# Kernel optimization log

Measured on AMD Instinct MI355X. Metric: run time of the kernel, lower is better.

Reference implementation:

```python
import math
import jax, jax.numpy as jnp
import numpy as np

D_MODEL = 1024
N_HEADS = 16
D_K = D_MODEL // N_HEADS
THETA = 10000.0
B, S = 2, 2048


def setup_inputs() -> dict:
    key = jax.random.key(0)
    k1, k2, k3 = jax.random.split(key, 3)
    x = jax.random.normal(k1, (B, S, D_MODEL), dtype=jnp.float32)
    token_positions = jnp.arange(B * S, dtype=jnp.int32).reshape(B, S)
    std_qkv = math.sqrt(2.0 / (D_MODEL + 3 * D_MODEL))
    std_o = math.sqrt(2.0 / (D_MODEL + D_MODEL))
    W_qkv = jax.random.truncated_normal(k2, -3.0, 3.0, (3 * D_MODEL, D_MODEL), dtype=jnp.float32) * std_qkv
    W_o = jax.random.truncated_normal(k3, -3.0, 3.0, (D_MODEL, D_MODEL), dtype=jnp.float32) * std_o
    return {"x": x, "W_qkv": W_qkv, "W_o": W_o, "token_positions": token_positions}


def _rope(x, pos):
    # x: (B, H, S, D_K); pos: (B, S) int
    half = D_K // 2
    inv_freq = 1.0 / (THETA ** (jnp.arange(0, D_K, 2, dtype=jnp.float32) / D_K))  # (half,)
    # pos_extended = pos[:, None, :] -> freqs (B, 1, S, half)
    freqs = pos[:, None, :, None].astype(jnp.float32) * inv_freq
    cos, sin = jnp.cos(freqs), jnp.sin(freqs)
    xr = x.reshape(*x.shape[:-1], half, 2)
    x1, x2 = xr[..., 0], xr[..., 1]
    out = jnp.stack([x1 * cos - x2 * sin, x2 * cos + x1 * sin], axis=-1)
    return out.reshape(x.shape)


def reference(x, W_qkv, W_o, token_positions):
    seq_len = x.shape[-2]
    qkv = jnp.einsum('bsi,oi->bso', x, W_qkv)
    q, k, v = jnp.split(qkv, 3, axis=-1)
    # (B, S, H*D) -> (B, H, S, D)
    def to_heads(t):
        return t.reshape(t.shape[0], t.shape[1], N_HEADS, D_K).transpose(0, 2, 1, 3)
    q, k, v = to_heads(q), to_heads(k), to_heads(v)
    q = _rope(q, token_positions)
    k = _rope(k, token_positions)
    scores = jnp.einsum('bhnd,bhmd->bhnm', q, k) / math.sqrt(D_K)
    causal = jnp.tril(jnp.ones((seq_len, seq_len), dtype=bool))
    scores = jnp.where(causal, scores, -jnp.inf)
    attn = jax.nn.softmax(scores, axis=-1)
    out = jnp.einsum('bhnm,bhmd->bhnd', attn, v)
    out = out.transpose(0, 2, 1, 3).reshape(x.shape[0], seq_len, D_MODEL)
    return jnp.einsum('bsi,oi->bso', out, W_o)
```

## Files before the change

### kernel.cpp

```cpp
#include <hip/hip_runtime.h>
#include <cmath>

typedef __bf16 bf16;
typedef bf16 bf16x4 __attribute__((ext_vector_type(4)));
typedef bf16 bf16x8 __attribute__((ext_vector_type(8)));
typedef float f32x4 __attribute__((ext_vector_type(4)));

#define MFMA16(a, b, c) __builtin_amdgcn_mfma_f32_16x16x32_bf16(a, b, c, 0, 0, 0)

__global__ __launch_bounds__(256) void cvt_all(
    const float* __restrict__ x, const float* __restrict__ wqkv,
    const float* __restrict__ wo, bf16* __restrict__ xb,
    bf16* __restrict__ wqkvb, bf16* __restrict__ wob) {
  int i = (blockIdx.x * 256 + threadIdx.x) * 4;
  const float* src;
  bf16* dst;
  if (i < (4 << 20)) {
    src = x + i; dst = xb + i;
  } else if (i < (7 << 20)) {
    src = wqkv + (i - (4 << 20)); dst = wqkvb + (i - (4 << 20));
  } else {
    src = wo + (i - (7 << 20)); dst = wob + (i - (7 << 20));
  }
  const f32x4 v = *(const f32x4*)src;
  bf16x4 o = {(bf16)v[0], (bf16)v[1], (bf16)v[2], (bf16)v[3]};
  *(bf16x4*)dst = o;
}

template <int EPI, int BN>
__global__ __launch_bounds__(256) void gemm_nt(
    const bf16* __restrict__ A, const bf16* __restrict__ Bm,
    const int* __restrict__ tokpos,
    bf16* __restrict__ out0, bf16* __restrict__ out1, bf16* __restrict__ out2,
    float* __restrict__ outF, int N) {
  constexpr int NI = BN / 32;
  __shared__ __align__(16) bf16 As[2][128 * 32];
  __shared__ __align__(16) bf16 Bs[2][BN * 32];
  const int tid = threadIdx.x;
  const int w = tid >> 6, lane = tid & 63, quad = lane >> 4, m16 = lane & 15;
  const int m0 = blockIdx.y * 128, n0 = blockIdx.x * BN;
  const int wm = (w >> 1) * 64, wn = (w & 1) * (BN / 2);

  f32x4 acc[4][NI] = {};

  const int row0 = tid >> 2, ch = tid & 3;
  const bf16* Ag0 = A + (size_t)(m0 + row0) * 1024 + ch * 8;
  const bf16* Ag1 = A + (size_t)(m0 + 64 + row0) * 1024 + ch * 8;
  const bf16* Bg0 = Bm + (size_t)(n0 + row0) * 1024 + ch * 8;
  const bf16* Bg1 =
      (BN == 128) ? Bm + (size_t)(n0 + 64 + row0) * 1024 + ch * 8 : nullptr;

  bf16x8 ra0, ra1, rb0, rb1;
  auto LOAD = [&](int k0) {
    ra0 = *(const bf16x8*)(Ag0 + k0);
    ra1 = *(const bf16x8*)(Ag1 + k0);
    rb0 = *(const bf16x8*)(Bg0 + k0);
    if constexpr (BN == 128) rb1 = *(const bf16x8*)(Bg1 + k0);
  };
  auto WRITE = [&](int p) {
    *(bf16x8*)(As[p] + tid * 8) = ra0;
    *(bf16x8*)(As[p] + 2048 + tid * 8) = ra1;
    *(bf16x8*)(Bs[p] + tid * 8) = rb0;
    if constexpr (BN == 128) *(bf16x8*)(Bs[p] + 2048 + tid * 8) = rb1;
  };

  LOAD(0);
  WRITE(0);
  __syncthreads();

  int p = 0;
  for (int k0 = 0; k0 < 1024; k0 += 32) {
    const bool more = (k0 + 32) < 1024;
    if (more) LOAD(k0 + 32);
    bf16x8 af[4], bfr[NI];
#pragma unroll
    for (int mi = 0; mi < 4; ++mi)
      af[mi] = *(const bf16x8*)(As[p] + (wm + mi * 16 + m16) * 32 + quad * 8);
#pragma unroll
    for (int ni = 0; ni < NI; ++ni)
      bfr[ni] = *(const bf16x8*)(Bs[p] + (wn + ni * 16 + m16) * 32 + quad * 8);
#pragma unroll
    for (int mi = 0; mi < 4; ++mi)
#pragma unroll
      for (int ni = 0; ni < NI; ++ni)
        acc[mi][ni] = MFMA16(af[mi], bfr[ni], acc[mi][ni]);
    if (more) {
      WRITE(1 - p);
      __syncthreads();
      p ^= 1;
    }
  }

  if constexpr (EPI == 0) {
#pragma unroll
    for (int mi = 0; mi < 4; ++mi) {
      int rowb = m0 + wm + mi * 16 + quad * 4;
#pragma unroll
      for (int r = 0; r < 4; ++r) {
        size_t off = (size_t)(rowb + r) * N + n0 + wn;
#pragma unroll
        for (int ni = 0; ni < NI; ++ni)
          outF[off + ni * 16 + m16] = acc[mi][ni][r];
      }
    }
  } else {
#pragma unroll
    for (int mi = 0; mi < 4; ++mi) {
      int rowb = m0 + wm + mi * 16 + quad * 4;
      int pos4[4];
#pragma unroll
      for (int r = 0; r < 4; ++r) pos4[r] = tokpos[rowb + r];
#pragma unroll
      for (int ni = 0; ni < NI; ++ni) {
        int col = n0 + wn + ni * 16 + m16;
        int sec = col >> 10, f = col & 1023, h = f >> 6, d = f & 63;
        if (sec == 2) {
#pragma unroll
          for (int r = 0; r < 4; ++r) {
            int row = rowb + r;
            int bb = row >> 11, s = row & 2047;
            out2[((size_t)(bb * 16 + h) * 64 + d) * 2048 + s] =
                (bf16)acc[mi][ni][r];
          }
        } else {
          float inv = __expf(-(float)(d & ~1) * (9.2103403719762f / 64.f));
          bf16* dst = sec ? out1 : out0;
          const float sc = sec ? 1.0f : 0.125f;
#pragma unroll
          for (int r = 0; r < 4; ++r) {
            float v = acc[mi][ni][r];
            float vp = __shfl_xor(v, 1);
            float ang = (float)pos4[r] * inv;
            float cs, sn;
            __sincosf(ang, &sn, &cs);
            float ov = (d & 1) ? (v * cs + vp * sn) : (v * cs - vp * sn);
            ov *= sc;
            int row = rowb + r;
            int bb = row >> 11, s = row & 2047;
            dst[((size_t)(bb * 16 + h) * 2048 + s) * 64 + d] = (bf16)ov;
          }
        }
      }
    }
  }
}

__global__ __launch_bounds__(256) void attn_kernel(
    const bf16* __restrict__ Q, const bf16* __restrict__ K,
    const bf16* __restrict__ Vt, bf16* __restrict__ O) {
  __shared__ __align__(16) bf16 KP[3][64 * 72];
  __shared__ __align__(16) bf16 VP[3][64 * 72];
  __shared__ __align__(16) bf16 PS[4][16 * 72];
  const int tid = threadIdx.x;
  const int w = tid >> 6, lane = tid & 63, quad = lane >> 4, m16 = lane & 15;
  const int bh = blockIdx.x;
  const int j = blockIdx.y;
  const int qtA = j, qtB = 31 - j;
  const int q0A = qtA * 64, q0B = qtB * 64;
  const bf16* Qb = Q + (size_t)bh * 2048 * 64;
  const bf16* Kb = K + (size_t)bh * 2048 * 64;
  const bf16* Vb = Vt + (size_t)bh * 64 * 2048;

  const int ch0 = w * 8, ch1 = (w + 4) * 8;
  const bf16* Kg = Kb + (size_t)lane * 64;
  const bf16* Vg = Vb + (size_t)lane * 2048;

  const bf16* qrowA = Qb + (size_t)(q0A + w * 16 + m16) * 64;
  const bf16* qrowB = Qb + (size_t)(q0B + w * 16 + m16) * 64;
  bf16x8 aqA[2], aqB[2];
  aqA[0] = *(const bf16x8*)(qrowA + quad * 8);
  aqA[1] = *(const bf16x8*)(qrowA + 32 + quad * 8);
  aqB[0] = *(const bf16x8*)(qrowB + quad * 8);
  aqB[1] = *(const bf16x8*)(qrowB + 32 + quad * 8);

  bf16x8 rk0, rk1, rv0, rv1;
  auto PREFETCH = [&](int kt) {
    rk0 = *(const bf16x8*)(Kg + (size_t)kt * 64 * 64 + ch0);
    rk1 = *(const bf16x8*)(Kg + (size_t)kt * 64 * 64 + ch1);
    rv0 = *(const bf16x8*)(Vg + kt * 64 + ch0);
    rv1 = *(const bf16x8*)(Vg + kt * 64 + ch1);
  };
  auto STAGE = [&](int p) {
    *(bf16x8*)(KP[p] + lane * 72 + ch0) = rk0;
    *(bf16x8*)(KP[p] + lane * 72 + ch1) = rk1;
    *(bf16x8*)(VP[p] + lane * 72 + ch0) = rv0;
    *(bf16x8*)(VP[p] + lane * 72 + ch1) = rv1;
  };

  PREFETCH(0);
  STAGE(0);
  PREFETCH(1);
  STAGE(1);
  __syncthreads();

  auto QK = [&](int p, const bf16x8* aq, f32x4* sa) {
#pragma unroll
    for (int kk = 0; kk < 2; ++kk)
#pragma unroll
      for (int ni = 0; ni < 4; ++ni) {
        bf16x8 bk = *(const bf16x8*)(KP[p] + (ni * 16 + m16) * 72 + kk * 32 +
                                     quad * 8);
        sa[ni] = MFMA16(aq[kk], bk, sa[ni]);
      }
  };

  f32x4 oA[4] = {}, oB[4] = {};
  float lA[4] = {0.f, 0.f, 0.f, 0.f}, lB[4] = {0.f, 0.f, 0.f, 0.f};
  const int qrel = w * 16 + quad * 4;

  auto SOFTPV = [&](int p, const f32x4* sa, f32x4* o, float* lp, bool diag) {
    bf16* ps = PS[w];
#pragma unroll
    for (int r = 0; r < 4; ++r) {
#pragma unroll
      for (int ni = 0; ni < 4; ++ni) {
        float pp = exp2f(fmaf(sa[ni][r], 1.44269504f, -11.5415603f));
        if (diag && (ni * 16 + m16) > qrel + r) pp = 0.f;
        lp[r] += pp;
        ps[(quad * 4 + r) * 72 + ni * 16 + m16] = (bf16)pp;
      }
    }
    bf16x8 ap[2];
    ap[0] = *(const bf16x8*)(ps + m16 * 72 + quad * 8);
    ap[1] = *(const bf16x8*)(ps + m16 * 72 + 32 + quad * 8);
#pragma unroll
    for (int kk = 0; kk < 2; ++kk)
#pragma unroll
      for (int ng = 0; ng < 4; ++ng) {
        bf16x8 bv = *(const bf16x8*)(VP[p] + (ng * 16 + m16) * 72 + kk * 32 +
                                     quad * 8);
        o[ng] = MFMA16(ap[kk], bv, o[ng]);
      }
  };

  f32x4 saA[4] = {}, saB[4] = {};
  QK(0, aqB, saB);
  QK(0, aqA, saA);

  int pc = 0, pn = 1, pst = 2;
  for (int kt = 0; kt <= qtB; ++kt) {
    const bool more = kt < qtB;
    const bool stage2 = (kt + 2) <= qtB;
    if (stage2) PREFETCH(kt + 2);

    f32x4 saBn[4] = {}, saAn[4] = {};
    if (more) QK(pn, aqB, saBn);
    if (kt + 1 <= qtA) QK(pn, aqA, saAn);

    SOFTPV(pc, saB, oB, lB, kt == qtB);
    if (kt <= qtA) SOFTPV(pc, saA, oA, lA, kt == qtA);

    if (stage2) STAGE(pst);
    if (more) __syncthreads();

#pragma unroll
    for (int i = 0; i < 4; ++i) { saB[i] = saBn[i]; saA[i] = saAn[i]; }
    int t = pc; pc = pn; pn = pst; pst = t;
  }

  const int b = bh >> 4, h = bh & 15;
  auto epilogue = [&](f32x4* o, float* lp, int q0) {
#pragma unroll
    for (int r = 0; r < 4; ++r) {
      float l = lp[r];
      l += __shfl_xor(l, 1);
      l += __shfl_xor(l, 2);
      l += __shfl_xor(l, 4);
      l += __shfl_xor(l, 8);
      float inv_l = 1.f / l;
      int s = q0 + w * 16 + quad * 4 + r;
      size_t rowoff = (size_t)(b * 2048 + s) * 1024 + h * 64;
#pragma unroll
      for (int ng = 0; ng < 4; ++ng)
        O[rowoff + ng * 16 + m16] = (bf16)(o[ng][r] * inv_l);
    }
  };
  epilogue(oA, lA, q0A);
  epilogue(oB, lB, q0B);
}

extern "C" void kernel_launch(void* const* d_in, const int* in_sizes, int n_in,
                              void* d_out, int out_size, void* d_ws, size_t ws_size,
                              hipStream_t stream) {
  (void)in_sizes; (void)n_in; (void)out_size; (void)ws_size;
  const float* x = (const float*)d_in[0];
  const float* Wqkv = (const float*)d_in[1];
  const float* Wo = (const float*)d_in[2];
  const int* tokpos = (const int*)d_in[3];
  float* out = (float*)d_out;

  const size_t NEL = (size_t)2 * 16 * 2048 * 64;
  bf16* Qws = (bf16*)d_ws;
  bf16* Kws = Qws + NEL;
  bf16* Vtw = Kws + NEL;
  bf16* Ows = Vtw + NEL;
  bf16* xb  = Ows + NEL;
  bf16* Wqkvb = xb + NEL;
  bf16* Wob = Wqkvb + (size_t)3072 * 1024;

  cvt_all<<<8192, 256, 0, stream>>>(x, Wqkv, Wo, xb, Wqkvb, Wob);

  gemm_nt<1, 128><<<dim3(24, 32), 256, 0, stream>>>(
      xb, Wqkvb, tokpos, Qws, Kws, Vtw, nullptr, 3072);
  attn_kernel<<<dim3(32, 16), 256, 0, stream>>>(Qws, Kws, Vtw, Ows);
  gemm_nt<0, 64><<<dim3(16, 32), 256, 0, stream>>>(
      Ows, Wob, nullptr, nullptr, nullptr, nullptr, out, 1024);
}
```

Measured before the change: 201.9 us.

## Split attention KV loop across two blocks and merge partials in output GEMM

Attention work is split by key tile parity (even/odd) across twice as many blocks, each writing unnormalized partial outputs and row sums. The output projection GEMM now loads both partials, sums them and divides by the combined row sum while staging A into shared memory, so the split-K merge is folded into the GEMM. V fragments are read directly from global memory into registers instead of through LDS, cutting shared memory and the K/V staging depth. Workspace buffers are aliased (xb and Wqkvb reused for the partials), which adds extra A-operand traffic and per-load divides in the GEMM.

```diff
diff --git a/kernel.cpp b/kernel.cpp
--- a/kernel.cpp
+++ b/kernel.cpp
@@ -29,7 +29,8 @@
 
 template <int EPI, int BN>
 __global__ __launch_bounds__(256) void gemm_nt(
-    const bf16* __restrict__ A, const bf16* __restrict__ Bm,
+    const bf16* __restrict__ A, const bf16* __restrict__ A2,
+    const float* __restrict__ lacc, const bf16* __restrict__ Bm,
     const int* __restrict__ tokpos,
     bf16* __restrict__ out0, bf16* __restrict__ out1, bf16* __restrict__ out2,
     float* __restrict__ outF, int N) {
@@ -46,20 +47,43 @@
   const int row0 = tid >> 2, ch = tid & 3;
   const bf16* Ag0 = A + (size_t)(m0 + row0) * 1024 + ch * 8;
   const bf16* Ag1 = A + (size_t)(m0 + 64 + row0) * 1024 + ch * 8;
+  const bf16* Cg0 = (EPI == 0) ? A2 + (size_t)(m0 + row0) * 1024 + ch * 8 : nullptr;
+  const bf16* Cg1 = (EPI == 0) ? A2 + (size_t)(m0 + 64 + row0) * 1024 + ch * 8 : nullptr;
   const bf16* Bg0 = Bm + (size_t)(n0 + row0) * 1024 + ch * 8;
   const bf16* Bg1 =
       (BN == 128) ? Bm + (size_t)(n0 + 64 + row0) * 1024 + ch * 8 : nullptr;
 
-  bf16x8 ra0, ra1, rb0, rb1;
+  bf16x8 ra0, ra1, rc0, rc1, rb0, rb1;
+  float lv0 = 1.f, lv1 = 1.f;
   auto LOAD = [&](int k0) {
     ra0 = *(const bf16x8*)(Ag0 + k0);
     ra1 = *(const bf16x8*)(Ag1 + k0);
+    if constexpr (EPI == 0) {
+      rc0 = *(const bf16x8*)(Cg0 + k0);
+      rc1 = *(const bf16x8*)(Cg1 + k0);
+      int h2 = ((k0 + ch * 8) >> 6) * 2;
+      lv0 = lacc[(m0 + row0) * 32 + h2] + lacc[(m0 + row0) * 32 + h2 + 1];
+      lv1 = lacc[(m0 + 64 + row0) * 32 + h2] +
+            lacc[(m0 + 64 + row0) * 32 + h2 + 1];
+    }
     rb0 = *(const bf16x8*)(Bg0 + k0);
     if constexpr (BN == 128) rb1 = *(const bf16x8*)(Bg1 + k0);
   };
   auto WRITE = [&](int p) {
-    *(bf16x8*)(As[p] + tid * 8) = ra0;
-    *(bf16x8*)(As[p] + 2048 + tid * 8) = ra1;
+    if constexpr (EPI == 0) {
+      float i0 = 1.f / lv0, i1 = 1.f / lv1;
+      bf16x8 w0, w1;
+#pragma unroll
+      for (int t = 0; t < 8; ++t) {
+        w0[t] = (bf16)(((float)ra0[t] + (float)rc0[t]) * i0);
+        w1[t] = (bf16)(((float)ra1[t] + (float)rc1[t]) * i1);
+      }
+      *(bf16x8*)(As[p] + tid * 8) = w0;
+      *(bf16x8*)(As[p] + 2048 + tid * 8) = w1;
+    } else {
+      *(bf16x8*)(As[p] + tid * 8) = ra0;
+      *(bf16x8*)(As[p] + 2048 + tid * 8) = ra1;
+    }
     *(bf16x8*)(Bs[p] + tid * 8) = rb0;
     if constexpr (BN == 128) *(bf16x8*)(Bs[p] + 2048 + tid * 8) = rb1;
   };
@@ -147,23 +171,23 @@
 
 __global__ __launch_bounds__(256) void attn_kernel(
     const bf16* __restrict__ Q, const bf16* __restrict__ K,
-    const bf16* __restrict__ Vt, bf16* __restrict__ O) {
-  __shared__ __align__(16) bf16 KP[3][64 * 72];
-  __shared__ __align__(16) bf16 VP[3][64 * 72];
+    const bf16* __restrict__ Vt, bf16* __restrict__ O0,
+    bf16* __restrict__ O1, float* __restrict__ lbuf) {
+  __shared__ __align__(16) bf16 KP[2][64 * 72];
   __shared__ __align__(16) bf16 PS[4][16 * 72];
   const int tid = threadIdx.x;
   const int w = tid >> 6, lane = tid & 63, quad = lane >> 4, m16 = lane & 15;
   const int bh = blockIdx.x;
-  const int j = blockIdx.y;
+  const int wk = blockIdx.y;
+  const int j = wk & 15, khalf = wk >> 4;
   const int qtA = j, qtB = 31 - j;
   const int q0A = qtA * 64, q0B = qtB * 64;
   const bf16* Qb = Q + (size_t)bh * 2048 * 64;
   const bf16* Kb = K + (size_t)bh * 2048 * 64;
-  const bf16* Vb = Vt + (size_t)bh * 64 * 2048;
 
   const int ch0 = w * 8, ch1 = (w + 4) * 8;
   const bf16* Kg = Kb + (size_t)lane * 64;
-  const bf16* Vg = Vb + (size_t)lane * 2048;
+  const bf16* Vfrag = Vt + (size_t)bh * 64 * 2048 + m16 * 2048 + quad * 8;
 
   const bf16* qrowA = Qb + (size_t)(q0A + w * 16 + m16) * 64;
   const bf16* qrowB = Qb + (size_t)(q0B + w * 16 + m16) * 64;
@@ -173,92 +197,80 @@
   aqB[0] = *(const bf16x8*)(qrowB + quad * 8);
   aqB[1] = *(const bf16x8*)(qrowB + 32 + quad * 8);
 
-  bf16x8 rk0, rk1, rv0, rv1;
-  auto PREFETCH = [&](int kt) {
+  bf16x8 rk0, rk1;
+  auto PREFETCHK = [&](int kt) {
     rk0 = *(const bf16x8*)(Kg + (size_t)kt * 64 * 64 + ch0);
     rk1 = *(const bf16x8*)(Kg + (size_t)kt * 64 * 64 + ch1);
-    rv0 = *(const bf16x8*)(Vg + kt * 64 + ch0);
-    rv1 = *(const bf16x8*)(Vg + kt * 64 + ch1);
   };
   auto STAGE = [&](int p) {
     *(bf16x8*)(KP[p] + lane * 72 + ch0) = rk0;
     *(bf16x8*)(KP[p] + lane * 72 + ch1) = rk1;
-    *(bf16x8*)(VP[p] + lane * 72 + ch0) = rv0;
-    *(bf16x8*)(VP[p] + lane * 72 + ch1) = rv1;
-  };
-
-  PREFETCH(0);
+  };
+
+  PREFETCHK(khalf);
   STAGE(0);
-  PREFETCH(1);
-  STAGE(1);
   __syncthreads();
-
-  auto QK = [&](int p, const bf16x8* aq, f32x4* sa) {
-#pragma unroll
-    for (int kk = 0; kk < 2; ++kk)
-#pragma unroll
-      for (int ni = 0; ni < 4; ++ni) {
-        bf16x8 bk = *(const bf16x8*)(KP[p] + (ni * 16 + m16) * 72 + kk * 32 +
-                                     quad * 8);
-        sa[ni] = MFMA16(aq[kk], bk, sa[ni]);
-      }
-  };
 
   f32x4 oA[4] = {}, oB[4] = {};
   float lA[4] = {0.f, 0.f, 0.f, 0.f}, lB[4] = {0.f, 0.f, 0.f, 0.f};
   const int qrel = w * 16 + quad * 4;
 
-  auto SOFTPV = [&](int p, const f32x4* sa, f32x4* o, float* lp, bool diag) {
-    bf16* ps = PS[w];
-#pragma unroll
-    for (int r = 0; r < 4; ++r) {
-#pragma unroll
-      for (int ni = 0; ni < 4; ++ni) {
-        float pp = exp2f(fmaf(sa[ni][r], 1.44269504f, -11.5415603f));
-        if (diag && (ni * 16 + m16) > qrel + r) pp = 0.f;
-        lp[r] += pp;
-        ps[(quad * 4 + r) * 72 + ni * 16 + m16] = (bf16)pp;
+  int p = 0;
+  for (int kt = khalf; kt <= qtB; kt += 2) {
+    const bool more = (kt + 2) <= qtB;
+    if (more) PREFETCHK(kt + 2);
+
+    bf16x8 bv[2][4];
+#pragma unroll
+    for (int kk = 0; kk < 2; ++kk)
+#pragma unroll
+      for (int ng = 0; ng < 4; ++ng)
+        bv[kk][ng] = *(const bf16x8*)(Vfrag + (size_t)ng * 16 * 2048 +
+                                      kt * 64 + kk * 32);
+
+    auto strip = [&](const bf16x8* aq, f32x4* o, float* lp, bool diag) {
+      f32x4 sa[4] = {};
+#pragma unroll
+      for (int kk = 0; kk < 2; ++kk)
+#pragma unroll
+        for (int ni = 0; ni < 4; ++ni) {
+          bf16x8 bk = *(const bf16x8*)(KP[p] + (ni * 16 + m16) * 72 +
+                                       kk * 32 + quad * 8);
+          sa[ni] = MFMA16(aq[kk], bk, sa[ni]);
+        }
+      bf16* ps = PS[w];
+#pragma unroll
+      for (int r = 0; r < 4; ++r) {
+#pragma unroll
+        for (int ni = 0; ni < 4; ++ni) {
+          float pp = exp2f(fmaf(sa[ni][r], 1.44269504f, -11.5415603f));
+          if (diag && (ni * 16 + m16) > qrel + r) pp = 0.f;
+          lp[r] += pp;
+          ps[(quad * 4 + r) * 72 + ni * 16 + m16] = (bf16)pp;
+        }
       }
-    }
-    bf16x8 ap[2];
-    ap[0] = *(const bf16x8*)(ps + m16 * 72 + quad * 8);
-    ap[1] = *(const bf16x8*)(ps + m16 * 72 + 32 + quad * 8);
-#pragma unroll
-    for (int kk = 0; kk < 2; ++kk)
-#pragma unroll
-      for (int ng = 0; ng < 4; ++ng) {
-        bf16x8 bv = *(const bf16x8*)(VP[p] + (ng * 16 + m16) * 72 + kk * 32 +
-                                     quad * 8);
-        o[ng] = MFMA16(ap[kk], bv, o[ng]);
-      }
-  };
-
-  f32x4 saA[4] = {}, saB[4] = {};
-  QK(0, aqB, saB);
-  QK(0, aqA, saA);
-
-  int pc = 0, pn = 1, pst = 2;
-  for (int kt = 0; kt <= qtB; ++kt) {
-    const bool more = kt < qtB;
-    const bool stage2 = (kt + 2) <= qtB;
-    if (stage2) PREFETCH(kt + 2);
-
-    f32x4 saBn[4] = {}, saAn[4] = {};
-    if (more) QK(pn, aqB, saBn);
-    if (kt + 1 <= qtA) QK(pn, aqA, saAn);
-
-    SOFTPV(pc, saB, oB, lB, kt == qtB);
-    if (kt <= qtA) SOFTPV(pc, saA, oA, lA, kt == qtA);
-
-    if (stage2) STAGE(pst);
-    if (more) __syncthreads();
-
-#pragma unroll
-    for (int i = 0; i < 4; ++i) { saB[i] = saBn[i]; saA[i] = saAn[i]; }
-    int t = pc; pc = pn; pn = pst; pst = t;
+      bf16x8 ap[2];
+      ap[0] = *(const bf16x8*)(ps + m16 * 72 + quad * 8);
+      ap[1] = *(const bf16x8*)(ps + m16 * 72 + 32 + quad * 8);
+#pragma unroll
+      for (int kk = 0; kk < 2; ++kk)
+#pragma unroll
+        for (int ng = 0; ng < 4; ++ng)
+          o[ng] = MFMA16(ap[kk], bv[kk][ng], o[ng]);
+    };
+
+    strip(aqB, oB, lB, kt == qtB);
+    if (kt <= qtA) strip(aqA, oA, lA, kt == qtA);
+
+    if (more) {
+      STAGE(1 - p);
+      __syncthreads();
+      p ^= 1;
+    }
   }
 
   const int b = bh >> 4, h = bh & 15;
+  bf16* Ob = khalf ? O1 : O0;
   auto epilogue = [&](f32x4* o, float* lp, int q0) {
 #pragma unroll
     for (int r = 0; r < 4; ++r) {
@@ -267,12 +279,12 @@
       l += __shfl_xor(l, 2);
       l += __shfl_xor(l, 4);
       l += __shfl_xor(l, 8);
-      float inv_l = 1.f / l;
       int s = q0 + w * 16 + quad * 4 + r;
       size_t rowoff = (size_t)(b * 2048 + s) * 1024 + h * 64;
 #pragma unroll
       for (int ng = 0; ng < 4; ++ng)
-        O[rowoff + ng * 16 + m16] = (bf16)(o[ng][r] * inv_l);
+        Ob[rowoff + ng * 16 + m16] = (bf16)o[ng][r];
+      if (m16 == 0) lbuf[(size_t)(b * 2048 + s) * 32 + h * 2 + khalf] = l;
     }
   };
   epilogue(oA, lA, q0A);
@@ -289,20 +301,22 @@
   const int* tokpos = (const int*)d_in[3];
   float* out = (float*)d_out;
 
-  const size_t NEL = (size_t)2 * 16 * 2048 * 64;
-  bf16* Qws = (bf16*)d_ws;
-  bf16* Kws = Qws + NEL;
-  bf16* Vtw = Kws + NEL;
-  bf16* Ows = Vtw + NEL;
-  bf16* xb  = Ows + NEL;
-  bf16* Wqkvb = xb + NEL;
-  bf16* Wob = Wqkvb + (size_t)3072 * 1024;
+  char* wsb = (char*)d_ws;
+  bf16* Qws = (bf16*)wsb;
+  bf16* Kws = (bf16*)(wsb + ((size_t)8 << 20));
+  bf16* Vtw = (bf16*)(wsb + ((size_t)16 << 20));
+  bf16* xb = (bf16*)(wsb + ((size_t)24 << 20));
+  bf16* O0 = (bf16*)(wsb + ((size_t)24 << 20));
+  bf16* Wqkvb = (bf16*)(wsb + ((size_t)32 << 20));
+  bf16* O1 = (bf16*)(wsb + ((size_t)32 << 20));
+  float* lbuf = (float*)(wsb + ((size_t)40 << 20));
+  bf16* Wob = (bf16*)(wsb + ((size_t)40 << 20) + ((size_t)512 << 10));
 
   cvt_all<<<8192, 256, 0, stream>>>(x, Wqkv, Wo, xb, Wqkvb, Wob);
 
   gemm_nt<1, 128><<<dim3(24, 32), 256, 0, stream>>>(
-      xb, Wqkvb, tokpos, Qws, Kws, Vtw, nullptr, 3072);
-  attn_kernel<<<dim3(32, 16), 256, 0, stream>>>(Qws, Kws, Vtw, Ows);
+      xb, nullptr, nullptr, Wqkvb, tokpos, Qws, Kws, Vtw, nullptr, 3072);
+  attn_kernel<<<dim3(32, 32), 256, 0, stream>>>(Qws, Kws, Vtw, O0, O1, lbuf);
   gemm_nt<0, 64><<<dim3(16, 32), 256, 0, stream>>>(
-      Ows, Wob, nullptr, nullptr, nullptr, nullptr, out, 1024);
+      O0, O1, lbuf, Wob, nullptr, nullptr, nullptr, nullptr, out, 1024);
 }
```

Measured after the change: 234.5 us. 16.1% more time.
